# Kernel optimization log

Hardware: AMD Instinct MI355X
Metric: run time of the kernel (lower is better)

Reference implementation:

```python
import jax, jax.numpy as jnp
import numpy as np

B, DIM, H, W = 8, 256, 128, 128
P = 4               # patch_size
HEADS = 8
HD = DIM // HEADS   # head dim = 32
CPB_HIDDEN = 512    # hidden width of the dynamic RPE MLP


def setup_inputs() -> dict:
    key = jax.random.key(0)
    ks = jax.random.split(key, 12)
    s = 0.02
    return {
        "x": jax.random.normal(ks[0], (B, DIM, H, W), dtype=jnp.float32),
        # PatchEmbed2d: Conv2d(dim, dim, kernel=P, stride=P)  weight [O, I, P, P]
        "w_embed": jax.random.normal(ks[1], (DIM, DIM, P, P), dtype=jnp.float32) * s,
        "b_embed": jnp.zeros((DIM,), dtype=jnp.float32),
        # DynamicPosEncoder: MLP(2 -> CPB_HIDDEN -> HEADS) on relative coords
        "cpb_w1": jax.random.normal(ks[2], (CPB_HIDDEN, 2), dtype=jnp.float32) * s,
        "cpb_b1": jnp.zeros((CPB_HIDDEN,), dtype=jnp.float32),
        "cpb_w2": jax.random.normal(ks[3], (HEADS, CPB_HIDDEN), dtype=jnp.float32) * s,
        # MaskAttention2d
        "w_qkv": jax.random.normal(ks[4], (3 * DIM, DIM), dtype=jnp.float32) * s,
        "b_qkv": jnp.zeros((3 * DIM,), dtype=jnp.float32),
        "w_proj": jax.random.normal(ks[5], (DIM, DIM), dtype=jnp.float32) * s,
        "b_proj": jnp.zeros((DIM,), dtype=jnp.float32),
        # PatchUnEmbed2d: ConvTranspose2d(dim, dim, kernel=P, stride=P)  weight [I, O, P, P]
        "w_unembed": jax.random.normal(ks[6], (DIM, DIM, P, P), dtype=jnp.float32) * s,
        "b_unembed": jnp.zeros((DIM,), dtype=jnp.float32),
    }


def _rpe_bias(Hp, Wp, cpb_w1, cpb_b1, cpb_w2):
    """Dynamic relative position bias -> [HEADS, N, N], N = Hp*Wp."""
    # continuous relative-coordinate table [(2Hp-1)*(2Wp-1), 2], normalized to [-1, 1]
    rh = (jnp.arange(2 * Hp - 1, dtype=jnp.float32) - (Hp - 1)) / max(Hp - 1, 1)
    rw = (jnp.arange(2 * Wp - 1, dtype=jnp.float32) - (Wp - 1)) / max(Wp - 1, 1)
    rel = jnp.stack(jnp.meshgrid(rh, rw, indexing="ij"), axis=-1).reshape(-1, 2)
    table = jax.nn.relu(rel @ cpb_w1.T + cpb_b1) @ cpb_w2.T  # [(2Hp-1)(2Wp-1), HEADS]
    # static relative position index [N, N]
    ch = np.arange(Hp)
    cw = np.arange(Wp)
    coords = np.stack(np.meshgrid(ch, cw, indexing="ij")).reshape(2, -1)  # [2, N]
    d = coords[:, :, None] - coords[:, None, :]                           # [2, N, N]
    idx = (d[0] + Hp - 1) * (2 * Wp - 1) + (d[1] + Wp - 1)               # [N, N]
    bias = table[jnp.asarray(idx)]                                        # [N, N, HEADS]
    return bias.transpose(2, 0, 1)                                        # [HEADS, N, N]


def reference(x, w_embed, b_embed, cpb_w1, cpb_b1, cpb_w2,
              w_qkv, b_qkv, w_proj, b_proj, w_unembed, b_unembed):
    Bx, C, Hf, Wf = x.shape
    Hp, Wp = Hf // P, Wf // P
    N = Hp * Wp
    # ---- patch embed: Conv2d(k=P, s=P) as block reshape + einsum ----
    xr = x.reshape(Bx, C, Hp, P, Wp, P)
    z = jnp.einsum("bchpwq,ocpq->bohw", xr, w_embed) + b_embed[None, :, None, None]
    # ---- dynamic RPE bias ----
    bias = _rpe_bias(Hp, Wp, cpb_w1, cpb_b1, cpb_w2)  # [HEADS, N, N]
    # ---- multi-head self-attention over the Hp*Wp grid ----
    tok = z.reshape(Bx, C, N).transpose(0, 2, 1)                     # [B, N, C]
    qkv = tok @ w_qkv.T + b_qkv                                       # [B, N, 3C]
    qkv = qkv.reshape(Bx, N, 3, HEADS, HD).transpose(2, 0, 3, 1, 4)   # [3, B, H, N, hd]
    q, k, v = qkv[0], qkv[1], qkv[2]
    scale = HD ** -0.5
    attn = jnp.einsum("bhnd,bhmd->bhnm", q * scale, k) + bias[None]   # [B, H, N, N]
    attn = jax.nn.softmax(attn, axis=-1)
    out = jnp.einsum("bhnm,bhmd->bhnd", attn, v)                      # [B, H, N, hd]
    out = out.transpose(0, 2, 1, 3).reshape(Bx, N, C)
    out = out @ w_proj.T + b_proj                                     # [B, N, C]
    z2 = out.transpose(0, 2, 1).reshape(Bx, C, Hp, Wp)
    # ---- patch unembed: ConvTranspose2d(k=P, s=P) as einsum + block reshape ----
    y = jnp.einsum("bchw,copq->bohpwq", z2, w_unembed)
    y = y.reshape(Bx, C, Hf, Wf) + b_unembed[None, :, None, None]
    return y
```

## Files before the change

kernel.cpp:

```cpp
#include <hip/hip_runtime.h>
#include <cstdint>
#include <cstddef>


typedef __bf16 bf16x8 __attribute__((ext_vector_type(8)));
typedef float f32x4 __attribute__((ext_vector_type(4)));
typedef unsigned short u16x4 __attribute__((ext_vector_type(4)));

__device__ __forceinline__ unsigned short f2bf(float f) {
  unsigned u = __builtin_bit_cast(unsigned, f);
  u += 0x7fffu + ((u >> 16) & 1u);
  return (unsigned short)(u >> 16);
}
__device__ __forceinline__ float bf2f(unsigned short u) {
  return __builtin_bit_cast(float, ((unsigned)u) << 16);
}

__device__ __forceinline__ void async_ld16(const void* g, void* l) {
  __builtin_amdgcn_global_load_lds(
      (const __attribute__((address_space(1))) void*)g,
      (__attribute__((address_space(3))) void*)l, 16, 0, 0);
}

__device__ __forceinline__ bf16x8 cvt8f(float4 a, float4 b) {
  unsigned short t[8] = {f2bf(a.x), f2bf(a.y), f2bf(a.z), f2bf(a.w),
                         f2bf(b.x), f2bf(b.y), f2bf(b.z), f2bf(b.w)};
  return *(const bf16x8*)t;
}

__global__ __launch_bounds__(256) void rpe_table_kernel(
    const float* __restrict__ w1, const float* __restrict__ b1,
    const float* __restrict__ w2, float* __restrict__ tableT) {
  int t = blockIdx.x * 256 + threadIdx.x;
  if (t >= 3969) return;
  int a = t / 63, c = t - a * 63;
  float rh = (float)(a - 31) * (1.0f / 31.0f);
  float rw = (float)(c - 31) * (1.0f / 31.0f);
  float acc[8];
#pragma unroll
  for (int h = 0; h < 8; h++) acc[h] = 0.f;
  for (int j = 0; j < 512; j++) {
    float hv = fmaxf(rh * w1[2 * j] + rw * w1[2 * j + 1] + b1[j], 0.f);
#pragma unroll
    for (int h = 0; h < 8; h++) acc[h] += hv * w2[h * 512 + j];
  }
#pragma unroll
  for (int h = 0; h < 8; h++) tableT[h * 4096 + t] = acc[h];
}

__global__ __launch_bounds__(256) void cvt_bf16_kernel(
    const float* __restrict__ src, unsigned short* __restrict__ dst, int n8) {
  int i = blockIdx.x * 256 + threadIdx.x;
  if (i >= n8) return;
  const float4* s4 = (const float4*)src + (size_t)i * 2;
  float4 a = s4[0], b = s4[1];
  unsigned short t[8] = {f2bf(a.x), f2bf(a.y), f2bf(a.z), f2bf(a.w),
                         f2bf(b.x), f2bf(b.y), f2bf(b.z), f2bf(b.w)};
  *(uint4*)(dst + (size_t)i * 8) = *(const uint4*)t;
}

__global__ __launch_bounds__(256) void transpose_cvt_kernel(
    const float* __restrict__ src, unsigned short* __restrict__ dst) {
  __shared__ float tile[32][33];
  int bx = blockIdx.x;
  int by = blockIdx.y;
  int tx = threadIdx.x & 31, ty = threadIdx.x >> 5;
#pragma unroll
  for (int r = 0; r < 32; r += 8)
    tile[ty + r][tx] = src[(size_t)(by * 32 + ty + r) * 4096 + bx * 32 + tx];
  __syncthreads();
#pragma unroll
  for (int r = 0; r < 32; r += 8)
    dst[(size_t)(bx * 32 + ty + r) * 256 + by * 32 + tx] = f2bf(tile[tx][ty + r]);
}

template <int NS>
__global__ __launch_bounds__(256) void splitk_reduce_kernel(
    const float* __restrict__ part, const float* __restrict__ bias,
    unsigned short* __restrict__ out) {
  size_t i = ((size_t)blockIdx.x * 256 + threadIdx.x) * 8;
  const float4* p = (const float4*)(part + i);
  const size_t s4 = 2097152 / 4;
  float4 a0 = p[0], a1 = p[1];
#pragma unroll
  for (int s = 1; s < NS; s++) {
    float4 b0 = p[s * s4], b1 = p[s * s4 + 1];
    a0.x += b0.x; a0.y += b0.y; a0.z += b0.z; a0.w += b0.w;
    a1.x += b1.x; a1.y += b1.y; a1.z += b1.z; a1.w += b1.w;
  }
  int col = (int)(i & 255);
  unsigned short t8[8] = {
      f2bf(a0.x + bias[col + 0]), f2bf(a0.y + bias[col + 1]),
      f2bf(a0.z + bias[col + 2]), f2bf(a0.w + bias[col + 3]),
      f2bf(a1.x + bias[col + 4]), f2bf(a1.y + bias[col + 5]),
      f2bf(a1.z + bias[col + 6]), f2bf(a1.w + bias[col + 7])};
  *(uint4*)(out + i) = *(const uint4*)t8;
}

__global__ __launch_bounds__(256) void gemm_embed_kernel(
    const float* __restrict__ x, const unsigned short* __restrict__ Bw,
    float* __restrict__ Cpart) {
  __shared__ unsigned short Bs[2 * 4096];
  int tid = threadIdx.x;
  int lane = tid & 63, wave = tid >> 6;

  int L = blockIdx.x;
  int xcd = L & 7, j = L >> 3;
  int pair = xcd * 32 + (j >> 1);
  int n0 = (j & 1) * 128;
  int z = pair & 3, y = pair >> 2;
  int m0 = y * 128;
  int wm = (wave & 1) * 64, wn = (wave >> 1) * 64;
  int fr = lane & 15, fh = lane >> 4;

  f32x4 acc[4][4];
#pragma unroll
  for (int i = 0; i < 4; i++)
#pragma unroll
    for (int jj = 0; jj < 4; jj++) acc[i][jj] = (f32x4){0.f, 0.f, 0.f, 0.f};

  int f0 = tid, f1 = tid + 256;
  const unsigned short* Bg0 =
      Bw + (size_t)(n0 + (f0 >> 2)) * 4096 + z * 1024 + (f0 & 3) * 8;
  const unsigned short* Bg1 =
      Bw + (size_t)(n0 + (f1 >> 2)) * 4096 + z * 1024 + (f1 & 3) * 8;
  unsigned short* Bl0 = Bs + f0 * 8;
  unsigned short* Bl1 = Bs + f1 * 8;

  const float4* x4 = (const float4*)x;
  int c0 = z * 64 + (fh >> 1);
  int p0 = (fh * 2) & 3;
  const float4* xp[4];
#pragma unroll
  for (int tt = 0; tt < 4; tt++) {
    int m = m0 + wm + tt * 16 + fr;
    int b_ = m >> 10, hp = (m >> 5) & 31, wp = m & 31;
    xp[tt] = x4 + (size_t)((b_ * 256 + c0) * 128 + hp * 4 + p0) * 32 + wp;
  }

  float4 aC[8], aN[8];

  async_ld16(Bg0, Bl0);
  async_ld16(Bg1, Bl1);
#pragma unroll
  for (int tt = 0; tt < 4; tt++) {
    aC[2 * tt] = xp[tt][0];
    aC[2 * tt + 1] = xp[tt][32];
  }
#pragma unroll
  for (int tt = 0; tt < 4; tt++) {
    aN[2 * tt] = xp[tt][8192];
    aN[2 * tt + 1] = xp[tt][8224];
  }
  asm volatile("s_waitcnt vmcnt(16) lgkmcnt(0)\n\ts_barrier" ::: "memory");

  auto step = [&](int t, float4 (&aCur)[8]) {
    bf16x8 af[4];
#pragma unroll
    for (int tt = 0; tt < 4; tt++)
      af[tt] = cvt8f(aCur[2 * tt], aCur[2 * tt + 1]);
    const unsigned short* Bsc = Bs + ((t & 1) << 12);
    bf16x8 bfr[4];
#pragma unroll
    for (int tt = 0; tt < 4; tt++)
      bfr[tt] = *(const bf16x8*)(Bsc + (wn + tt * 16 + fr) * 32 + fh * 8);
    int tb = (t + 1 > 31) ? 31 : t + 1;
    async_ld16(Bg0 + (tb << 5), Bl0 + (((t + 1) & 1) << 12));
    async_ld16(Bg1 + (tb << 5), Bl1 + (((t + 1) & 1) << 12));
    int tc = (t + 2 > 31) ? 31 : t + 2;
    size_t ax = (size_t)tc * 8192;
#pragma unroll
    for (int tt = 0; tt < 4; tt++) {
      aCur[2 * tt] = xp[tt][ax];
      aCur[2 * tt + 1] = xp[tt][ax + 32];
    }
    __builtin_amdgcn_s_setprio(1);
#pragma unroll
    for (int mt = 0; mt < 4; mt++)
#pragma unroll
      for (int nt = 0; nt < 4; nt++)
        acc[mt][nt] = __builtin_amdgcn_mfma_f32_16x16x32_bf16(
            af[mt], bfr[nt], acc[mt][nt], 0, 0, 0);
    __builtin_amdgcn_s_setprio(0);
    asm volatile("s_waitcnt vmcnt(8) lgkmcnt(0)\n\ts_barrier" ::: "memory");
  };

  for (int it = 0; it < 16; it++) {
    step(2 * it, aC);
    step(2 * it + 1, aN);
  }

  float* Cp = Cpart + (size_t)z * 2097152;
#pragma unroll
  for (int mt = 0; mt < 4; mt++) {
    int row0 = m0 + wm + mt * 16 + fh * 4;
#pragma unroll
    for (int nt = 0; nt < 4; nt++) {
      int col = n0 + wn + nt * 16 + fr;
#pragma unroll
      for (int r = 0; r < 4; r++)
        Cp[(size_t)(row0 + r) * 256 + col] = acc[mt][nt][r];
    }
  }
}

template <int CMODE>
__global__ __launch_bounds__(256) void gemm_mfma_kernel(
    const unsigned short* __restrict__ A, const unsigned short* __restrict__ B,
    const float* __restrict__ bias, void* __restrict__ Cv,
    int M, int N, int K, int lda, int ldb, int ldc) {
  __shared__ unsigned short As[2 * 128 * 32];
  __shared__ unsigned short Bs[2 * 128 * 32];
  int tid = threadIdx.x;
  int lane = tid & 63;
  int wave = tid >> 6;
  int m0 = blockIdx.y * 128, n0 = blockIdx.x * 128;
  int wm = (wave & 1) * 64, wn = (wave >> 1) * 64;

  if (CMODE == 4) {
    int s = blockIdx.z;
    A += (size_t)s * K;
    B += (size_t)s * K;
    Cv = (void*)((float*)Cv + (size_t)s * M * N);
  }

  f32x4 acc[4][4];
#pragma unroll
  for (int i = 0; i < 4; i++)
#pragma unroll
    for (int j = 0; j < 4; j++) acc[i][j] = (f32x4){0.f, 0.f, 0.f, 0.f};

  int f0 = tid, f1 = tid + 256;
  const unsigned short* Ag0 = A + (size_t)(m0 + (f0 >> 2)) * lda + (f0 & 3) * 8;
  const unsigned short* Ag1 = A + (size_t)(m0 + (f1 >> 2)) * lda + (f1 & 3) * 8;
  const unsigned short* Bg0 = B + (size_t)(n0 + (f0 >> 2)) * ldb + (f0 & 3) * 8;
  const unsigned short* Bg1 = B + (size_t)(n0 + (f1 >> 2)) * ldb + (f1 & 3) * 8;
  unsigned short* Al0 = As + f0 * 8;
  unsigned short* Al1 = As + f1 * 8;
  unsigned short* Bl0 = Bs + f0 * 8;
  unsigned short* Bl1 = Bs + f1 * 8;

  int fr = lane & 15;
  int fh = lane >> 4;

  int ntiles = K >> 5;
  async_ld16(Ag0, Al0);
  async_ld16(Ag1, Al1);
  async_ld16(Bg0, Bl0);
  async_ld16(Bg1, Bl1);
  __syncthreads();

  for (int t = 0; t < ntiles; t++) {
    int cur = (t & 1) << 12;
    int nxt = cur ^ 4096;
    if (t + 1 < ntiles) {
      int kn = (t + 1) << 5;
      async_ld16(Ag0 + kn, Al0 + nxt);
      async_ld16(Ag1 + kn, Al1 + nxt);
      async_ld16(Bg0 + kn, Bl0 + nxt);
      async_ld16(Bg1 + kn, Bl1 + nxt);
    }
    const unsigned short* Asc = As + cur;
    const unsigned short* Bsc = Bs + cur;
    bf16x8 af[4], bfr[4];
#pragma unroll
    for (int tt = 0; tt < 4; tt++) {
      af[tt] = *(const bf16x8*)(Asc + (wm + tt * 16 + fr) * 32 + fh * 8);
      bfr[tt] = *(const bf16x8*)(Bsc + (wn + tt * 16 + fr) * 32 + fh * 8);
    }
#pragma unroll
    for (int mt = 0; mt < 4; mt++)
#pragma unroll
      for (int nt = 0; nt < 4; nt++)
        acc[mt][nt] = __builtin_amdgcn_mfma_f32_16x16x32_bf16(
            af[mt], bfr[nt], acc[mt][nt], 0, 0, 0);
    __syncthreads();
  }

#pragma unroll
  for (int mt = 0; mt < 4; mt++) {
    int row0 = m0 + wm + mt * 16 + fh * 4;
    if (CMODE == 2) {
      int b = row0 >> 10, hp = (row0 >> 5) & 31, wp = row0 & 31;
      size_t rowoff0 = (size_t)b * 4194304 + hp * 512 + wp * 4;
      float* y = (float*)Cv;
#pragma unroll
      for (int nt = 0; nt < 4; nt++) {
        int col = n0 + wn + nt * 16 + fr;
        int o = col >> 4, p = (col >> 2) & 3, q = col & 3;
        size_t coloff = (size_t)o * 16384 + p * 128 + q;
        float bv = bias[o];
#pragma unroll
        for (int r = 0; r < 4; r++)
          y[rowoff0 + r * 4 + coloff] = acc[mt][nt][r] + bv;
      }
    } else if (CMODE == 3) {
      unsigned short* base = (unsigned short*)Cv;
#pragma unroll
      for (int nt = 0; nt < 4; nt++) {
        int col = n0 + wn + nt * 16 + fr;
        int which = col >> 8, hh = (col >> 5) & 7, d = col & 31;
        float bv = bias[col];
#pragma unroll
        for (int r = 0; r < 4; r++) {
          int row = row0 + r;
          int bb = row >> 10, nn = row & 1023;
          int bh = bb * 8 + hh;
          float v = acc[mt][nt][r] + bv;
          if (which == 0) v *= 0.17677669529663687f;
          size_t addr;
          if (which < 2)
            addr = (size_t)which * 2097152 + ((size_t)bh * 1024 + nn) * 32 + d;
          else
            addr = (size_t)2 * 2097152 + (size_t)bh * 32768 + (size_t)d * 1024 + nn;
          base[addr] = f2bf(v);
        }
      }
    } else if (CMODE == 4) {
      float* Cp = (float*)Cv;
#pragma unroll
      for (int nt = 0; nt < 4; nt++) {
        int col = n0 + wn + nt * 16 + fr;
#pragma unroll
        for (int r = 0; r < 4; r++)
          Cp[(size_t)(row0 + r) * ldc + col] = acc[mt][nt][r];
      }
    } else {
#pragma unroll
      for (int nt = 0; nt < 4; nt++) {
        int col = n0 + wn + nt * 16 + fr;
        float bv = bias ? bias[col] : 0.f;
        unsigned short* C = (unsigned short*)Cv;
#pragma unroll
        for (int r = 0; r < 4; r++)
          C[(size_t)(row0 + r) * ldc + col] = f2bf(acc[mt][nt][r] + bv);
      }
    }
  }
}

__global__ __launch_bounds__(512) void attn_mfma_kernel(
    const unsigned short* __restrict__ Qb, const unsigned short* __restrict__ Kb,
    const unsigned short* __restrict__ Vtb,
    const float* __restrict__ tableT,
    unsigned short* __restrict__ out) {
  __shared__ float th[3972];
  __shared__ unsigned short Ps[2][8][1088];

  int tid = threadIdx.x;
  int lane = tid & 63, w = tid >> 6;
  int n = lane & 15, g = lane >> 4;
  int blk = blockIdx.x;
  int h = blk & 7, b = (blk >> 3) & 7, qt = blk >> 6;
  int bh = b * 8 + h;
  int q0 = qt * 128;

  const unsigned short* Qg = Qb + ((size_t)bh * 1024 + q0) * 32;
  const unsigned short* Kg = Kb + (size_t)bh * 1024 * 32;
  const unsigned short* Vg = Vtb + (size_t)bh * 32 * 1024;
  const float* tg = tableT + (size_t)h * 4096;

  for (int i = tid; i < 3969; i += 512) th[i] = tg[i];
  bf16x8 qf = *(const bf16x8*)(Qg + (size_t)(w * 16 + n) * 32 + g * 8);
  __syncthreads();

  f32x4 oacc[2];
  oacc[0] = (f32x4){0.f, 0.f, 0.f, 0.f};
  oacc[1] = (f32x4){0.f, 0.f, 0.f, 0.f};
  float m_run = -1e30f, l_run = 0.f;

  int q = q0 + w * 16 + n;
  int tbase = (q >> 5) * 63 + (q & 31) + 1984;

  unsigned short* PwA = &Ps[0][w][0];
  unsigned short* PwB = &Ps[1][w][0];

  bf16x8 kfA[4], kfB[4];
#pragma unroll
  for (int mt = 0; mt < 4; mt++)
    kfA[mt] = *(const bf16x8*)(Kg + (size_t)(mt * 16 + n) * 32 + g * 8);

  auto half_step = [&](const bf16x8 (&kf)[4], int k0, unsigned short* Pw) {
    bf16x8 vf[4];
#pragma unroll
    for (int i = 0; i < 4; i++)
      vf[i] = *(const bf16x8*)(Vg + (size_t)((i & 1) * 16 + n) * 1024 + k0 +
                               (i >> 1) * 32 + g * 8);

    f32x4 s[4];
    __builtin_amdgcn_s_setprio(1);
#pragma unroll
    for (int mt = 0; mt < 4; mt++)
      s[mt] = __builtin_amdgcn_mfma_f32_16x16x32_bf16(
          kf[mt], qf, (f32x4){0.f, 0.f, 0.f, 0.f}, 0, 0, 0);
    __builtin_amdgcn_s_setprio(0);

#pragma unroll
    for (int mt = 0; mt < 4; mt++) {
      int kb = k0 + mt * 16 + g * 4;
      int ib = tbase - (kb >> 5) * 63 - (kb & 31);
      s[mt][0] += th[ib];
      s[mt][1] += th[ib - 1];
      s[mt][2] += th[ib - 2];
      s[mt][3] += th[ib - 3];
    }

    float mx = -1e30f;
#pragma unroll
    for (int mt = 0; mt < 4; mt++)
#pragma unroll
      for (int r = 0; r < 4; r++) mx = fmaxf(mx, s[mt][r]);
    mx = fmaxf(mx, __shfl_xor(mx, 16, 64));
    mx = fmaxf(mx, __shfl_xor(mx, 32, 64));
    float m_new = fmaxf(m_run, mx);
    float alpha = __expf(m_run - m_new);
    m_run = m_new;

    float ls = 0.f;
#pragma unroll
    for (int mt = 0; mt < 4; mt++) {
#pragma unroll
      for (int r = 0; r < 4; r++) {
        float p = __expf(s[mt][r] - m_new);
        s[mt][r] = p;
        ls += p;
      }
      u16x4 pk = {f2bf(s[mt][0]), f2bf(s[mt][1]), f2bf(s[mt][2]),
                  f2bf(s[mt][3])};
      *(u16x4*)(Pw + n * 68 + mt * 16 + g * 4) = pk;
    }
    l_run = l_run * alpha + ls;

#pragma unroll
    for (int dt = 0; dt < 2; dt++)
#pragma unroll
      for (int r = 0; r < 4; r++) oacc[dt][r] *= alpha;
    __builtin_amdgcn_s_setprio(1);
#pragma unroll
    for (int kt = 0; kt < 2; kt++) {
      bf16x8 pf = *(const bf16x8*)(Pw + n * 68 + kt * 32 + g * 8);
      oacc[0] = __builtin_amdgcn_mfma_f32_16x16x32_bf16(vf[kt * 2 + 0], pf,
                                                        oacc[0], 0, 0, 0);
      oacc[1] = __builtin_amdgcn_mfma_f32_16x16x32_bf16(vf[kt * 2 + 1], pf,
                                                        oacc[1], 0, 0, 0);
    }
    __builtin_amdgcn_s_setprio(0);
  };

  for (int tt = 0; tt < 8; tt++) {
    int k0 = tt * 128;
#pragma unroll
    for (int mt = 0; mt < 4; mt++)
      kfB[mt] = *(const bf16x8*)(Kg + (size_t)(k0 + 64 + mt * 16 + n) * 32 +
                                 g * 8);
    half_step(kfA, k0, PwA);
    if (tt < 7) {
#pragma unroll
      for (int mt = 0; mt < 4; mt++)
        kfA[mt] = *(const bf16x8*)(Kg + (size_t)(k0 + 128 + mt * 16 + n) * 32 +
                                   g * 8);
    }
    half_step(kfB, k0 + 64, PwB);
  }

  float l = l_run;
  l += __shfl_xor(l, 16, 64);
  l += __shfl_xor(l, 32, 64);
  float invl = 1.f / l;
  unsigned short* ob = out + ((size_t)(b * 1024 + q) * 256) + h * 32;
#pragma unroll
  for (int dt = 0; dt < 2; dt++) {
    u16x4 o4 = {f2bf(oacc[dt][0] * invl), f2bf(oacc[dt][1] * invl),
                f2bf(oacc[dt][2] * invl), f2bf(oacc[dt][3] * invl)};
    *(u16x4*)(ob + dt * 16 + g * 4) = o4;
  }
}

extern "C" void kernel_launch(void* const* d_in, const int* in_sizes, int n_in,
                              void* d_out, int out_size, void* d_ws, size_t ws_size,
                              hipStream_t stream) {
  const float* x         = (const float*)d_in[0];
  const float* w_embed   = (const float*)d_in[1];
  const float* b_embed   = (const float*)d_in[2];
  const float* cpb_w1    = (const float*)d_in[3];
  const float* cpb_b1    = (const float*)d_in[4];
  const float* cpb_w2    = (const float*)d_in[5];
  const float* w_qkv     = (const float*)d_in[6];
  const float* b_qkv     = (const float*)d_in[7];
  const float* w_proj    = (const float*)d_in[8];
  const float* b_proj    = (const float*)d_in[9];
  const float* w_unembed = (const float*)d_in[10];
  const float* b_unembed = (const float*)d_in[11];
  float* out = (float*)d_out;

  char* w = (char*)d_ws;
  float*          ProjP = (float*)w;          w += (size_t)8388608 * 4;
  unsigned short* tok   = (unsigned short*)w; w += (size_t)8192 * 256 * 2;
  unsigned short* wE    = (unsigned short*)w; w += (size_t)1048576 * 2;
  unsigned short* wQ    = (unsigned short*)w; w += (size_t)196608 * 2;
  unsigned short* wP    = (unsigned short*)w; w += (size_t)65536 * 2;
  unsigned short* wUt   = (unsigned short*)w; w += (size_t)1048576 * 2;
  float*          tableT= (float*)w;          w += (size_t)32768 * 4;
  float*          PART  = (float*)w;          w += (size_t)4 * 2097152 * 4;

  unsigned short* qkvB  = (unsigned short*)PART;
  unsigned short* attno = (unsigned short*)((char*)PART + 12582912);
  unsigned short* z2    = (unsigned short*)((char*)PART + 16777216);
  unsigned short* Qb  = qkvB;
  unsigned short* Kb  = qkvB + 2097152;
  unsigned short* Vtb = qkvB + 2 * 2097152;

  cvt_bf16_kernel<<<512, 256, 0, stream>>>(w_embed, wE, 131072);
  cvt_bf16_kernel<<<96, 256, 0, stream>>>(w_qkv, wQ, 24576);
  cvt_bf16_kernel<<<32, 256, 0, stream>>>(w_proj, wP, 8192);
  transpose_cvt_kernel<<<dim3(128, 8), 256, 0, stream>>>(w_unembed, wUt);
  rpe_table_kernel<<<16, 256, 0, stream>>>(cpb_w1, cpb_b1, cpb_w2, tableT);

  gemm_embed_kernel<<<512, 256, 0, stream>>>(x, wE, PART);
  splitk_reduce_kernel<4><<<1024, 256, 0, stream>>>(PART, b_embed, tok);

  gemm_mfma_kernel<3><<<dim3(6, 64), 256, 0, stream>>>(
      tok, wQ, b_qkv, qkvB, 8192, 768, 256, 256, 256, 0);

  attn_mfma_kernel<<<512, 512, 0, stream>>>(Qb, Kb, Vtb, tableT, attno);

  gemm_mfma_kernel<4><<<dim3(2, 64, 4), 256, 0, stream>>>(
      attno, wP, nullptr, ProjP, 8192, 256, 64, 256, 256, 256);
  splitk_reduce_kernel<4><<<1024, 256, 0, stream>>>(ProjP, b_proj, z2);

  gemm_mfma_kernel<2><<<dim3(32, 64), 256, 0, stream>>>(
      z2, wUt, b_unembed, out, 8192, 4096, 256, 256, 256, 0);
}
```

Measured before the change: 486.7 us.

## Fold projection into unembed weights, merge prep kernels, deepen embed pipeline, lazy softmax rescale

The output projection is folded algebraically into the unembed weights (Wc = Wu^T·Wp^T with a combined bias). This removes the split-K projection GEMM and its reduce pass, and the unembed GEMM now consumes the attention output directly. The weight conversions and the RPE table are merged into one prep kernel. The embed GEMM gains a triple-buffered prefetch of one more stage. The attention softmax skips the running-max rescale unless the max rises by more than a threshold. The weight product is computed in bf16, which adds rounding error, and the deeper prefetch uses more registers and LDS.

```diff
diff --git a/kernel.cpp b/kernel.cpp
--- a/kernel.cpp
+++ b/kernel.cpp
@@ -12,9 +12,6 @@
   u += 0x7fffu + ((u >> 16) & 1u);
   return (unsigned short)(u >> 16);
 }
-__device__ __forceinline__ float bf2f(unsigned short u) {
-  return __builtin_bit_cast(float, ((unsigned)u) << 16);
-}
 
 __device__ __forceinline__ void async_ld16(const void* g, void* l) {
   __builtin_amdgcn_global_load_lds(
@@ -28,50 +25,71 @@
   return *(const bf16x8*)t;
 }
 
-__global__ __launch_bounds__(256) void rpe_table_kernel(
-    const float* __restrict__ w1, const float* __restrict__ b1,
-    const float* __restrict__ w2, float* __restrict__ tableT) {
-  int t = blockIdx.x * 256 + threadIdx.x;
-  if (t >= 3969) return;
-  int a = t / 63, c = t - a * 63;
-  float rh = (float)(a - 31) * (1.0f / 31.0f);
-  float rw = (float)(c - 31) * (1.0f / 31.0f);
-  float acc[8];
-#pragma unroll
-  for (int h = 0; h < 8; h++) acc[h] = 0.f;
-  for (int j = 0; j < 512; j++) {
-    float hv = fmaxf(rh * w1[2 * j] + rw * w1[2 * j + 1] + b1[j], 0.f);
-#pragma unroll
-    for (int h = 0; h < 8; h++) acc[h] += hv * w2[h * 512 + j];
-  }
-#pragma unroll
-  for (int h = 0; h < 8; h++) tableT[h * 4096 + t] = acc[h];
-}
-
-__global__ __launch_bounds__(256) void cvt_bf16_kernel(
-    const float* __restrict__ src, unsigned short* __restrict__ dst, int n8) {
-  int i = blockIdx.x * 256 + threadIdx.x;
-  if (i >= n8) return;
-  const float4* s4 = (const float4*)src + (size_t)i * 2;
-  float4 a = s4[0], b = s4[1];
-  unsigned short t[8] = {f2bf(a.x), f2bf(a.y), f2bf(a.z), f2bf(a.w),
-                         f2bf(b.x), f2bf(b.y), f2bf(b.z), f2bf(b.w)};
-  *(uint4*)(dst + (size_t)i * 8) = *(const uint4*)t;
-}
-
-__global__ __launch_bounds__(256) void transpose_cvt_kernel(
-    const float* __restrict__ src, unsigned short* __restrict__ dst) {
+__global__ __launch_bounds__(256) void prep_kernel(
+    const float* __restrict__ w_embed, const float* __restrict__ w_qkv,
+    const float* __restrict__ w_unembed, const float* __restrict__ w_proj,
+    const float* __restrict__ cpb_w1, const float* __restrict__ cpb_b1,
+    const float* __restrict__ cpb_w2, const float* __restrict__ b_proj,
+    const float* __restrict__ b_unembed,
+    unsigned short* __restrict__ wE, unsigned short* __restrict__ wQ,
+    unsigned short* __restrict__ wUt, unsigned short* __restrict__ wPT,
+    float* __restrict__ tableT, float* __restrict__ bc) {
   __shared__ float tile[32][33];
-  int bx = blockIdx.x;
-  int by = blockIdx.y;
-  int tx = threadIdx.x & 31, ty = threadIdx.x >> 5;
-#pragma unroll
-  for (int r = 0; r < 32; r += 8)
-    tile[ty + r][tx] = src[(size_t)(by * 32 + ty + r) * 4096 + bx * 32 + tx];
-  __syncthreads();
-#pragma unroll
-  for (int r = 0; r < 32; r += 8)
-    dst[(size_t)(bx * 32 + ty + r) * 256 + by * 32 + tx] = f2bf(tile[tx][ty + r]);
+  int bx = blockIdx.x, tid = threadIdx.x;
+
+  if (bx < 608) {
+    const float* src = (bx < 512) ? w_embed : w_qkv;
+    unsigned short* dst = (bx < 512) ? wE : wQ;
+    int i = (bx < 512) ? bx * 256 + tid : (bx - 512) * 256 + tid;
+    const float4* s4 = (const float4*)src + (size_t)i * 2;
+    float4 a = s4[0], b = s4[1];
+    unsigned short t[8] = {f2bf(a.x), f2bf(a.y), f2bf(a.z), f2bf(a.w),
+                           f2bf(b.x), f2bf(b.y), f2bf(b.z), f2bf(b.w)};
+    *(uint4*)(dst + (size_t)i * 8) = *(const uint4*)t;
+  } else if (bx < 1696) {
+    const float* src;
+    unsigned short* dst;
+    int C, bx2, by2;
+    if (bx < 1632) {
+      src = w_unembed; dst = wUt; C = 4096;
+      int idx = bx - 608; bx2 = idx & 127; by2 = idx >> 7;
+    } else {
+      src = w_proj; dst = wPT; C = 256;
+      int idx = bx - 1632; bx2 = idx & 7; by2 = idx >> 3;
+    }
+    int tx = tid & 31, ty = tid >> 5;
+#pragma unroll
+    for (int r = 0; r < 32; r += 8)
+      tile[ty + r][tx] = src[(size_t)(by2 * 32 + ty + r) * C + bx2 * 32 + tx];
+    __syncthreads();
+#pragma unroll
+    for (int r = 0; r < 32; r += 8)
+      dst[(size_t)(bx2 * 32 + ty + r) * 256 + by2 * 32 + tx] =
+          f2bf(tile[tx][ty + r]);
+  } else if (bx < 1712) {
+    int t = (bx - 1696) * 256 + tid;
+    if (t >= 3969) return;
+    int a = t / 63, c = t - a * 63;
+    float rh = (float)(a - 31) * (1.0f / 31.0f);
+    float rw = (float)(c - 31) * (1.0f / 31.0f);
+    float acc[8];
+#pragma unroll
+    for (int h = 0; h < 8; h++) acc[h] = 0.f;
+    for (int j = 0; j < 512; j++) {
+      float hv = fmaxf(rh * cpb_w1[2 * j] + rw * cpb_w1[2 * j + 1] + cpb_b1[j],
+                       0.f);
+#pragma unroll
+      for (int h = 0; h < 8; h++) acc[h] += hv * cpb_w2[h * 512 + j];
+    }
+#pragma unroll
+    for (int h = 0; h < 8; h++) tableT[h * 4096 + t] = acc[h];
+  } else {
+    int j = (bx - 1712) * 256 + tid;
+    float s = 0.f;
+#pragma unroll 4
+    for (int c = 0; c < 256; c++) s += b_proj[c] * w_unembed[(size_t)c * 4096 + j];
+    bc[j] = s + b_unembed[j >> 4];
+  }
 }
 
 template <int NS>
@@ -100,7 +118,7 @@
 __global__ __launch_bounds__(256) void gemm_embed_kernel(
     const float* __restrict__ x, const unsigned short* __restrict__ Bw,
     float* __restrict__ Cpart) {
-  __shared__ unsigned short Bs[2 * 4096];
+  __shared__ unsigned short Bs[3 * 4096];
   int tid = threadIdx.x;
   int lane = tid & 63, wave = tid >> 6;
 
@@ -138,42 +156,44 @@
     xp[tt] = x4 + (size_t)((b_ * 256 + c0) * 128 + hp * 4 + p0) * 32 + wp;
   }
 
-  float4 aC[8], aN[8];
+  float4 aA[8], aB[8], aC[8];
+
+#define LOADX(areg, T)                                  \
+  {                                                     \
+    size_t ax_ = (size_t)(T)*8192;                      \
+    _Pragma("unroll") for (int tt = 0; tt < 4; tt++) {  \
+      areg[2 * tt] = xp[tt][ax_];                       \
+      areg[2 * tt + 1] = xp[tt][ax_ + 32];              \
+    }                                                   \
+  }
 
   async_ld16(Bg0, Bl0);
   async_ld16(Bg1, Bl1);
-#pragma unroll
-  for (int tt = 0; tt < 4; tt++) {
-    aC[2 * tt] = xp[tt][0];
-    aC[2 * tt + 1] = xp[tt][32];
-  }
-#pragma unroll
-  for (int tt = 0; tt < 4; tt++) {
-    aN[2 * tt] = xp[tt][8192];
-    aN[2 * tt + 1] = xp[tt][8224];
-  }
-  asm volatile("s_waitcnt vmcnt(16) lgkmcnt(0)\n\ts_barrier" ::: "memory");
+  LOADX(aA, 0);
+  asm volatile("" ::: "memory");
+  async_ld16(Bg0 + 32, Bl0 + 4096);
+  async_ld16(Bg1 + 32, Bl1 + 4096);
+  LOADX(aB, 1);
+  asm volatile("" ::: "memory");
+  LOADX(aC, 2);
+  asm volatile("s_waitcnt vmcnt(18) lgkmcnt(0)\n\ts_barrier" ::: "memory");
 
   auto step = [&](int t, float4 (&aCur)[8]) {
     bf16x8 af[4];
 #pragma unroll
     for (int tt = 0; tt < 4; tt++)
       af[tt] = cvt8f(aCur[2 * tt], aCur[2 * tt + 1]);
-    const unsigned short* Bsc = Bs + ((t & 1) << 12);
+    const unsigned short* Bsc = Bs + (t % 3) * 4096;
     bf16x8 bfr[4];
 #pragma unroll
     for (int tt = 0; tt < 4; tt++)
       bfr[tt] = *(const bf16x8*)(Bsc + (wn + tt * 16 + fr) * 32 + fh * 8);
-    int tb = (t + 1 > 31) ? 31 : t + 1;
-    async_ld16(Bg0 + (tb << 5), Bl0 + (((t + 1) & 1) << 12));
-    async_ld16(Bg1 + (tb << 5), Bl1 + (((t + 1) & 1) << 12));
-    int tc = (t + 2 > 31) ? 31 : t + 2;
-    size_t ax = (size_t)tc * 8192;
-#pragma unroll
-    for (int tt = 0; tt < 4; tt++) {
-      aCur[2 * tt] = xp[tt][ax];
-      aCur[2 * tt + 1] = xp[tt][ax + 32];
-    }
+    int tb = (t + 2 > 31) ? 31 : t + 2;
+    async_ld16(Bg0 + (tb << 5), Bl0 + (tb % 3) * 4096);
+    async_ld16(Bg1 + (tb << 5), Bl1 + (tb % 3) * 4096);
+    asm volatile("" ::: "memory");
+    int tc = (t + 3 > 31) ? 31 : t + 3;
+    LOADX(aCur, tc);
     __builtin_amdgcn_s_setprio(1);
 #pragma unroll
     for (int mt = 0; mt < 4; mt++)
@@ -182,13 +202,17 @@
         acc[mt][nt] = __builtin_amdgcn_mfma_f32_16x16x32_bf16(
             af[mt], bfr[nt], acc[mt][nt], 0, 0, 0);
     __builtin_amdgcn_s_setprio(0);
-    asm volatile("s_waitcnt vmcnt(8) lgkmcnt(0)\n\ts_barrier" ::: "memory");
+    asm volatile("s_waitcnt vmcnt(18) lgkmcnt(0)\n\ts_barrier" ::: "memory");
   };
 
-  for (int it = 0; it < 16; it++) {
-    step(2 * it, aC);
-    step(2 * it + 1, aN);
-  }
+  for (int it = 0; it < 10; it++) {
+    step(3 * it + 0, aA);
+    step(3 * it + 1, aB);
+    step(3 * it + 2, aC);
+  }
+  step(30, aA);
+  step(31, aB);
+#undef LOADX
 
   float* Cp = Cpart + (size_t)z * 2097152;
 #pragma unroll
@@ -289,7 +313,7 @@
         int col = n0 + wn + nt * 16 + fr;
         int o = col >> 4, p = (col >> 2) & 3, q = col & 3;
         size_t coloff = (size_t)o * 16384 + p * 128 + q;
-        float bv = bias[o];
+        float bv = bias[col];
 #pragma unroll
         for (int r = 0; r < 4; r++)
           y[rowoff0 + r * 4 + coloff] = acc[mt][nt][r] + bv;
@@ -412,16 +436,23 @@
       for (int r = 0; r < 4; r++) mx = fmaxf(mx, s[mt][r]);
     mx = fmaxf(mx, __shfl_xor(mx, 16, 64));
     mx = fmaxf(mx, __shfl_xor(mx, 32, 64));
-    float m_new = fmaxf(m_run, mx);
-    float alpha = __expf(m_run - m_new);
-    m_run = m_new;
+    if (!__all(mx <= m_run + 8.0f)) {
+      float m_new = fmaxf(m_run, mx);
+      float alpha = __expf(m_run - m_new);
+      m_run = m_new;
+      l_run *= alpha;
+#pragma unroll
+      for (int dt = 0; dt < 2; dt++)
+#pragma unroll
+        for (int r = 0; r < 4; r++) oacc[dt][r] *= alpha;
+    }
 
     float ls = 0.f;
 #pragma unroll
     for (int mt = 0; mt < 4; mt++) {
 #pragma unroll
       for (int r = 0; r < 4; r++) {
-        float p = __expf(s[mt][r] - m_new);
+        float p = __expf(s[mt][r] - m_run);
         s[mt][r] = p;
         ls += p;
       }
@@ -429,12 +460,8 @@
                   f2bf(s[mt][3])};
       *(u16x4*)(Pw + n * 68 + mt * 16 + g * 4) = pk;
     }
-    l_run = l_run * alpha + ls;
-
-#pragma unroll
-    for (int dt = 0; dt < 2; dt++)
-#pragma unroll
-      for (int r = 0; r < 4; r++) oacc[dt][r] *= alpha;
+    l_run += ls;
+
     __builtin_amdgcn_s_setprio(1);
 #pragma unroll
     for (int kt = 0; kt < 2; kt++) {
@@ -494,27 +521,28 @@
   float* out = (float*)d_out;
 
   char* w = (char*)d_ws;
-  float*          ProjP = (float*)w;          w += (size_t)8388608 * 4;
   unsigned short* tok   = (unsigned short*)w; w += (size_t)8192 * 256 * 2;
   unsigned short* wE    = (unsigned short*)w; w += (size_t)1048576 * 2;
   unsigned short* wQ    = (unsigned short*)w; w += (size_t)196608 * 2;
-  unsigned short* wP    = (unsigned short*)w; w += (size_t)65536 * 2;
   unsigned short* wUt   = (unsigned short*)w; w += (size_t)1048576 * 2;
+  unsigned short* wPT   = (unsigned short*)w; w += (size_t)65536 * 2;
+  unsigned short* Wc    = (unsigned short*)w; w += (size_t)1048576 * 2;
+  float*          bc    = (float*)w;          w += (size_t)4096 * 4;
   float*          tableT= (float*)w;          w += (size_t)32768 * 4;
   float*          PART  = (float*)w;          w += (size_t)4 * 2097152 * 4;
 
   unsigned short* qkvB  = (unsigned short*)PART;
   unsigned short* attno = (unsigned short*)((char*)PART + 12582912);
-  unsigned short* z2    = (unsigned short*)((char*)PART + 16777216);
   unsigned short* Qb  = qkvB;
   unsigned short* Kb  = qkvB + 2097152;
   unsigned short* Vtb = qkvB + 2 * 2097152;
 
-  cvt_bf16_kernel<<<512, 256, 0, stream>>>(w_embed, wE, 131072);
-  cvt_bf16_kernel<<<96, 256, 0, stream>>>(w_qkv, wQ, 24576);
-  cvt_bf16_kernel<<<32, 256, 0, stream>>>(w_proj, wP, 8192);
-  transpose_cvt_kernel<<<dim3(128, 8), 256, 0, stream>>>(w_unembed, wUt);
-  rpe_table_kernel<<<16, 256, 0, stream>>>(cpb_w1, cpb_b1, cpb_w2, tableT);
+  prep_kernel<<<1728, 256, 0, stream>>>(
+      w_embed, w_qkv, w_unembed, w_proj, cpb_w1, cpb_b1, cpb_w2, b_proj,
+      b_unembed, wE, wQ, wUt, wPT, tableT, bc);
+
+  gemm_mfma_kernel<1><<<dim3(2, 32), 256, 0, stream>>>(
+      wUt, wPT, nullptr, Wc, 4096, 256, 256, 256, 256, 256);
 
   gemm_embed_kernel<<<512, 256, 0, stream>>>(x, wE, PART);
   splitk_reduce_kernel<4><<<1024, 256, 0, stream>>>(PART, b_embed, tok);
@@ -524,10 +552,6 @@
 
   attn_mfma_kernel<<<512, 512, 0, stream>>>(Qb, Kb, Vtb, tableT, attno);
 
-  gemm_mfma_kernel<4><<<dim3(2, 64, 4), 256, 0, stream>>>(
-      attno, wP, nullptr, ProjP, 8192, 256, 64, 256, 256, 256);
-  splitk_reduce_kernel<4><<<1024, 256, 0, stream>>>(ProjP, b_proj, z2);
-
   gemm_mfma_kernel<2><<<dim3(32, 64), 256, 0, stream>>>(
-      z2, wUt, b_unembed, out, 8192, 4096, 256, 256, 256, 0);
-}
+      attno, Wc, bc, out, 8192, 4096, 256, 256, 256, 0);
+}
```

New measurement: 470.6 us. 3.3% less time.
